# Performance work log

Hardware: AMD Instinct MI355X
Metric: run time of the kernel (lower is better)

## Reference

```python
import jax, jax.numpy as jnp
import numpy as np

N = 8192
IN_F = 128
OUT_F = 128
ALPHA = 0.2  # LeakyReLU negative slope
NEG_INF = -9e15


def setup_inputs() -> dict:
    key = jax.random.key(0)
    k1, k2, k3, k4 = jax.random.split(key, 4)
    h = jax.random.normal(k1, (N, IN_F), dtype=jnp.float32)
    adj = jax.random.randint(k2, (N, N), 0, 2, dtype=jnp.int32)
    # nn.Linear(in, out, bias=False).weight is (out, in); store as (in, out) for h @ W
    W = jax.random.normal(k3, (IN_F, OUT_F), dtype=jnp.float32) * (1.0 / np.sqrt(IN_F))
    # a: (2*out_features, 1), xavier_uniform with gain=1.414
    limit = 1.414 * np.sqrt(6.0 / (2 * OUT_F + 1))
    a = jax.random.uniform(k4, (2 * OUT_F, 1), dtype=jnp.float32, minval=-limit, maxval=limit)
    return {"h": h, "adj": adj, "W": W, "a": a}


def reference(h, adj, W, a):
    Wh = h @ W  # (N, OUT_F)
    a1 = a[:OUT_F, 0]   # score contribution from source node i
    a2 = a[OUT_F:, 0]   # score contribution from target node j
    # e_ij = leakyrelu(Wh_i . a1 + Wh_j . a2) -- avoids the O(N^2 * 2F) concat
    s1 = Wh @ a1  # (N,)
    s2 = Wh @ a2  # (N,)
    e = jax.nn.leaky_relu(s1[:, None] + s2[None, :], negative_slope=ALPHA)  # (N, N)
    masked = jnp.where(adj > 0, e, NEG_INF)
    attention = jax.nn.softmax(masked, axis=1)  # (N, N)
    # dropout is a no-op in eval mode
    h_prime = attention @ Wh  # (N, OUT_F)
    return jax.nn.elu(h_prime)  # concat=True -> ELU
```

## Files before the change

### kernel.cpp

```cpp
#include <hip/hip_runtime.h>
#include <cstdint>
#include <cstddef>


#define NROW 8192
#define FDIM 128

typedef _Float16 f16;
typedef f16 f16x8 __attribute__((ext_vector_type(8)));
typedef float f32x4 __attribute__((ext_vector_type(4)));

#define WS_WHT 0u
#define WS_S12 (2u * 1024u * 1024u)
#define WS_RC  (WS_S12 + 64u * 1024u)
#define WS_EF  (WS_RC + 128u * 1024u)
#define WS_M2  (WS_EF + 64u * 1024u)

__global__ __launch_bounds__(256) void k1_wh(const float* __restrict__ h,
                                             const float* __restrict__ W,
                                             f16* __restrict__ WhT,
                                             unsigned* __restrict__ M2key) {
  __shared__ float hT[128 * 36];
  const int t = (int)threadIdx.x;
  const int rb = (int)blockIdx.x * 32;
  if (blockIdx.x == 0 && t == 0) *M2key = 0u;
  const f32x4* hv = (const f32x4*)(h + (size_t)rb * FDIM);
#pragma unroll
  for (int i = 0; i < 4; ++i) {
    int fidx = t + i * 256;
    f32x4 v = hv[fidx];
    int e0 = fidx * 4;
    int r = e0 >> 7, k = e0 & 127;
    hT[(k + 0) * 36 + r] = v[0];
    hT[(k + 1) * 36 + r] = v[1];
    hT[(k + 2) * 36 + r] = v[2];
    hT[(k + 3) * 36 + r] = v[3];
  }
  __syncthreads();
  const int f = t & 127, rh = t >> 7;
  f32x4 z = {0.f, 0.f, 0.f, 0.f};
  f32x4 acc0 = z, acc1 = z, acc2 = z, acc3 = z;
  for (int k = 0; k < 128; ++k) {
    float w = W[k * FDIM + f];
    const f32x4* hp = (const f32x4*)(hT + k * 36 + rh * 16);
    acc0 += hp[0] * w;
    acc1 += hp[1] * w;
    acc2 += hp[2] * w;
    acc3 += hp[3] * w;
  }
  union { f16 hx[16]; uint4 u[2]; } pk;
#pragma unroll
  for (int q = 0; q < 4; ++q) {
    pk.hx[0 + q]  = (f16)acc0[q];
    pk.hx[4 + q]  = (f16)acc1[q];
    pk.hx[8 + q]  = (f16)acc2[q];
    pk.hx[12 + q] = (f16)acc3[q];
  }
  uint4* dst = (uint4*)(WhT + (size_t)f * NROW + rb + rh * 16);
  dst[0] = pk.u[0];
  dst[1] = pk.u[1];
}

__global__ __launch_bounds__(256) void k1b_s(const f16* __restrict__ WhT,
                                             const float* __restrict__ a,
                                             float2* __restrict__ s12,
                                             unsigned* __restrict__ M2key) {
  int r = (int)blockIdx.x * 256 + (int)threadIdx.x;
  float s1 = 0.f, s2 = 0.f;
  for (int f = 0; f < 128; ++f) {
    float w = (float)WhT[(size_t)f * NROW + r];
    s1 = fmaf(w, a[f], s1);
    s2 = fmaf(w, a[128 + f], s2);
  }
  s12[r] = make_float2(s1, s2);
  float mx = s2;
#pragma unroll
  for (int off = 32; off; off >>= 1) mx = fmaxf(mx, __shfl_xor(mx, off, 64));
  if ((threadIdx.x & 63) == 0) {
    unsigned key = __float_as_uint(mx);
    key = (key & 0x80000000u) ? ~key : (key | 0x80000000u);
    atomicMax(M2key, key);
  }
}

__global__ __launch_bounds__(256) void k1c_prep(const float2* __restrict__ s12,
                                                const unsigned* __restrict__ M2key,
                                                float4* __restrict__ RC,
                                                float2* __restrict__ EF) {
  int j = (int)blockIdx.x * 256 + (int)threadIdx.x;
  unsigned key = *M2key;
  float M2 = (key & 0x80000000u) ? __uint_as_float(key ^ 0x80000000u)
                                 : __uint_as_float(~key);
  float2 s = s12[j];
  float c = s.x + M2;
  c = fmaxf(c, 0.2f * c);
  RC[j] = make_float4(__expf(-s.x), __expf(s.x - c), __expf(0.2f * s.x - c), 0.f);
  EF[j] = make_float2(__expf(s.y), __expf(0.2f * s.y));
}

__global__ __launch_bounds__(512) void k2_main(const int* __restrict__ adj,
                                               const f16* __restrict__ WhT,
                                               const float4* __restrict__ RC,
                                               const float* __restrict__ EF,
                                               float* __restrict__ out) {
  __shared__ __align__(16) f16 whbuf[2][8192];
  __shared__ float dpart[2][32];

  const int tid = (int)threadIdx.x;
  const int L = tid & 63, w = tid >> 6;
  const int mh = w & 1, kh = (w >> 1) & 1, nh = w >> 2;
  const int m = L & 15, kg = L >> 4;
  const int rb = (int)blockIdx.x * 32;
  const int rloc = mh * 16 + m;
  const int row = rb + rloc;
  const int jo = kh * 32 + kg * 8;

  const float4 rc = RC[row];
  const float tau = rc.x, kap1 = rc.y, kap2 = rc.z;

  const int sf0 = tid >> 3;
  const int scc = tid & 7;
  const int stl0 = sf0 * 64 + scc * 8;
  const f16* gp0 = WhT + (size_t)sf0 * NROW + (size_t)((scc ^ (sf0 & 7)) * 8);
  const f16* gp1 = gp0 + (size_t)64 * NROW;

  const int* ap = adj + (size_t)row * NROW + jo;
  const f32x4* ep = (const f32x4*)(EF + 2 * jo);

  uint4 S0 = *(const uint4*)gp0;
  uint4 S1 = *(const uint4*)gp1;
  int4 A0 = *(const int4*)ap;
  int4 A1 = *(const int4*)(ap + 4);
  f32x4 Ev0 = ep[0], Ev1 = ep[1], Ev2 = ep[2], Ev3 = ep[3];

  f32x4 z = {0.f, 0.f, 0.f, 0.f};
  f32x4 acc[4] = {z, z, z, z};
  float dloc = 0.f;

  const int bofs = (nh * 64 + m) * 64 + (((kh * 4 + kg) ^ (m & 7)) * 8);

  for (int t = 0; t < 128; ++t) {
    f16* wb = &whbuf[t & 1][0];
    *(uint4*)(wb + stl0) = S0;
    *(uint4*)(wb + stl0 + 4096) = S1;

    f16x8 af;
    {
      float p;
      p = (Ev0[0] > tau) ? Ev0[0] * kap1 : Ev0[1] * kap2; p = (A0.x > 0) ? p : 0.f; dloc += p; af[0] = (f16)p;
      p = (Ev0[2] > tau) ? Ev0[2] * kap1 : Ev0[3] * kap2; p = (A0.y > 0) ? p : 0.f; dloc += p; af[1] = (f16)p;
      p = (Ev1[0] > tau) ? Ev1[0] * kap1 : Ev1[1] * kap2; p = (A0.z > 0) ? p : 0.f; dloc += p; af[2] = (f16)p;
      p = (Ev1[2] > tau) ? Ev1[2] * kap1 : Ev1[3] * kap2; p = (A0.w > 0) ? p : 0.f; dloc += p; af[3] = (f16)p;
      p = (Ev2[0] > tau) ? Ev2[0] * kap1 : Ev2[1] * kap2; p = (A1.x > 0) ? p : 0.f; dloc += p; af[4] = (f16)p;
      p = (Ev2[2] > tau) ? Ev2[2] * kap1 : Ev2[3] * kap2; p = (A1.y > 0) ? p : 0.f; dloc += p; af[5] = (f16)p;
      p = (Ev3[0] > tau) ? Ev3[0] * kap1 : Ev3[1] * kap2; p = (A1.z > 0) ? p : 0.f; dloc += p; af[6] = (f16)p;
      p = (Ev3[2] > tau) ? Ev3[2] * kap1 : Ev3[3] * kap2; p = (A1.w > 0) ? p : 0.f; dloc += p; af[7] = (f16)p;
    }

    __syncthreads();

    int adv = (t < 127) ? 1 : 0;
    ap += adv * 64;
    ep += adv * 32;
    gp0 += adv * 64;
    gp1 += adv * 64;
    uint4 Sn0 = *(const uint4*)gp0;
    uint4 Sn1 = *(const uint4*)gp1;
    int4 An0 = *(const int4*)ap;
    int4 An1 = *(const int4*)(ap + 4);
    f32x4 En0 = ep[0], En1 = ep[1], En2 = ep[2], En3 = ep[3];

    const f16* wbB = wb + bofs;
    f16x8 b0 = *(const f16x8*)(wbB);
    f16x8 b1 = *(const f16x8*)(wbB + 1024);
    f16x8 b2 = *(const f16x8*)(wbB + 2048);
    f16x8 b3 = *(const f16x8*)(wbB + 3072);
    acc[0] = __builtin_amdgcn_mfma_f32_16x16x32_f16(af, b0, acc[0], 0, 0, 0);
    acc[1] = __builtin_amdgcn_mfma_f32_16x16x32_f16(af, b1, acc[1], 0, 0, 0);
    acc[2] = __builtin_amdgcn_mfma_f32_16x16x32_f16(af, b2, acc[2], 0, 0, 0);
    acc[3] = __builtin_amdgcn_mfma_f32_16x16x32_f16(af, b3, acc[3], 0, 0, 0);

    S0 = Sn0; S1 = Sn1; A0 = An0; A1 = An1;
    Ev0 = En0; Ev1 = En1; Ev2 = En2; Ev3 = En3;
  }

  dloc += __shfl_xor(dloc, 16, 64);
  dloc += __shfl_xor(dloc, 32, 64);
  if (nh == 0 && kg == 0) dpart[kh][rloc] = dloc;
  __syncthreads();

  float* red = (float*)&whbuf[0][0];
  const int q4 = (nh * 2 + mh) * 4;
  if (kh == 1) {
#pragma unroll
    for (int nt = 0; nt < 4; ++nt)
#pragma unroll
      for (int e = 0; e < 4; ++e)
        red[(q4 + nt) * 288 + (kg * 4 + e) * 18 + m] = acc[nt][e];
  }
  __syncthreads();
  if (kh == 0) {
    float inv0[4];
#pragma unroll
    for (int e = 0; e < 4; ++e) {
      int rr = mh * 16 + kg * 4 + e;
      inv0[e] = 1.0f / (dpart[0][rr] + dpart[1][rr]);
    }
#pragma unroll
    for (int nt = 0; nt < 4; ++nt) {
#pragma unroll
      for (int e = 0; e < 4; ++e) {
        float x = (acc[nt][e] + red[(q4 + nt) * 288 + (kg * 4 + e) * 18 + m]) * inv0[e];
        float r = x > 0.f ? x : expm1f(x);
        out[(size_t)(rb + mh * 16 + kg * 4 + e) * FDIM + nh * 64 + nt * 16 + m] = r;
      }
    }
  }
}

extern "C" void kernel_launch(void* const* d_in, const int* in_sizes, int n_in,
                              void* d_out, int out_size, void* d_ws, size_t ws_size,
                              hipStream_t stream) {
  const float* h = (const float*)d_in[0];
  const int* adj = (const int*)d_in[1];
  const float* W = (const float*)d_in[2];
  const float* a = (const float*)d_in[3];
  float* out = (float*)d_out;
  char* ws = (char*)d_ws;
  f16* WhT = (f16*)(ws + WS_WHT);
  float2* s12 = (float2*)(ws + WS_S12);
  float4* RC = (float4*)(ws + WS_RC);
  float2* EF = (float2*)(ws + WS_EF);
  unsigned* M2 = (unsigned*)(ws + WS_M2);

  k1_wh<<<dim3(256), dim3(256), 0, stream>>>(h, W, WhT, M2);
  k1b_s<<<dim3(32), dim3(256), 0, stream>>>(WhT, a, s12, M2);
  k1c_prep<<<dim3(32), dim3(256), 0, stream>>>(s12, M2, RC, EF);
  k2_main<<<dim3(256), dim3(512), 0, stream>>>(adj, WhT, RC, (const float*)EF, out);
}
```

Baseline: 533.2 us.

## Split-K main attention kernel over column chunks with 32x32 MFMA and combine pass

Rewrites the main attention-times-Wh kernel so each wavefront owns a 32-row block and one of S column chunks. It reads Wh from a pre-packed MFMA-ready fp16 layout straight from global memory instead of staging it through LDS with barriers, and uses 32x32x16 MFMAs. Partial numerators and denominators go to workspace and a new combine kernel normalizes them and applies ELU. This raises parallelism beyond 256 blocks and removes LDS sync, at the cost of partial-sum traffic, an extra launch and repeated global reads of the packed Wh. k1b_s is also split across four feature groups for more blocks.

Result: faster. 449.8 us (-15.6%).

```diff
diff --git a/kernel.cpp b/kernel.cpp
--- a/kernel.cpp
+++ b/kernel.cpp
@@ -9,16 +9,20 @@
 typedef _Float16 f16;
 typedef f16 f16x8 __attribute__((ext_vector_type(8)));
 typedef float f32x4 __attribute__((ext_vector_type(4)));
+typedef float f32x16 __attribute__((ext_vector_type(16)));
 
 #define WS_WHT 0u
-#define WS_S12 (2u * 1024u * 1024u)
-#define WS_RC  (WS_S12 + 64u * 1024u)
-#define WS_EF  (WS_RC + 128u * 1024u)
-#define WS_M2  (WS_EF + 64u * 1024u)
+#define WS_BP  (2u*1024u*1024u)
+#define WS_S12 (4u*1024u*1024u)
+#define WS_RC  (WS_S12 + 64u*1024u)
+#define WS_EF  (WS_RC + 128u*1024u)
+#define WS_M2  (WS_EF + 64u*1024u)
+#define WS_PWS (WS_M2 + 4u*1024u)
 
 __global__ __launch_bounds__(256) void k1_wh(const float* __restrict__ h,
                                              const float* __restrict__ W,
                                              f16* __restrict__ WhT,
+                                             f16* __restrict__ Bp,
                                              unsigned* __restrict__ M2key) {
   __shared__ float hT[128 * 36];
   const int t = (int)threadIdx.x;
@@ -59,27 +63,40 @@
   uint4* dst = (uint4*)(WhT + (size_t)f * NROW + rb + rh * 16);
   dst[0] = pk.u[0];
   dst[1] = pk.u[1];
+  f16* bdst = Bp + ((size_t)((blockIdx.x * 2 + rh) * 4 + (f >> 5)) * 64 + (f & 31)) * 8;
+  *(uint4*)bdst = pk.u[0];
+  *(uint4*)(bdst + 256) = pk.u[1];
 }
 
 __global__ __launch_bounds__(256) void k1b_s(const f16* __restrict__ WhT,
                                              const float* __restrict__ a,
                                              float2* __restrict__ s12,
                                              unsigned* __restrict__ M2key) {
-  int r = (int)blockIdx.x * 256 + (int)threadIdx.x;
+  __shared__ float part[2][4][64];
+  const int l = (int)threadIdx.x & 63;
+  const int fc = (int)threadIdx.x >> 6;
+  const int r = (int)blockIdx.x * 64 + l;
   float s1 = 0.f, s2 = 0.f;
-  for (int f = 0; f < 128; ++f) {
+  for (int f = fc * 32; f < fc * 32 + 32; ++f) {
     float w = (float)WhT[(size_t)f * NROW + r];
     s1 = fmaf(w, a[f], s1);
     s2 = fmaf(w, a[128 + f], s2);
   }
-  s12[r] = make_float2(s1, s2);
-  float mx = s2;
-#pragma unroll
-  for (int off = 32; off; off >>= 1) mx = fmaxf(mx, __shfl_xor(mx, off, 64));
-  if ((threadIdx.x & 63) == 0) {
-    unsigned key = __float_as_uint(mx);
-    key = (key & 0x80000000u) ? ~key : (key | 0x80000000u);
-    atomicMax(M2key, key);
+  part[0][fc][l] = s1;
+  part[1][fc][l] = s2;
+  __syncthreads();
+  if (fc == 0) {
+    s1 = part[0][0][l] + part[0][1][l] + part[0][2][l] + part[0][3][l];
+    s2 = part[1][0][l] + part[1][1][l] + part[1][2][l] + part[1][3][l];
+    s12[r] = make_float2(s1, s2);
+    float mx = s2;
+#pragma unroll
+    for (int off = 32; off; off >>= 1) mx = fmaxf(mx, __shfl_xor(mx, off, 64));
+    if (l == 0) {
+      unsigned key = __float_as_uint(mx);
+      key = (key & 0x80000000u) ? ~key : (key | 0x80000000u);
+      atomicMax(M2key, key);
+    }
   }
 }
 
@@ -98,124 +115,127 @@
   EF[j] = make_float2(__expf(s.y), __expf(0.2f * s.y));
 }
 
-__global__ __launch_bounds__(512) void k2_main(const int* __restrict__ adj,
-                                               const f16* __restrict__ WhT,
+__global__ __launch_bounds__(256) void k2_main(const int* __restrict__ adj,
+                                               const f16* __restrict__ Bp,
                                                const float4* __restrict__ RC,
                                                const float* __restrict__ EF,
-                                               float* __restrict__ out) {
-  __shared__ __align__(16) f16 whbuf[2][8192];
-  __shared__ float dpart[2][32];
-
+                                               float* __restrict__ Pws,
+                                               float* __restrict__ Dws,
+                                               int jspan) {
   const int tid = (int)threadIdx.x;
   const int L = tid & 63, w = tid >> 6;
-  const int mh = w & 1, kh = (w >> 1) & 1, nh = w >> 2;
-  const int m = L & 15, kg = L >> 4;
-  const int rb = (int)blockIdx.x * 32;
-  const int rloc = mh * 16 + m;
-  const int row = rb + rloc;
-  const int jo = kh * 32 + kg * 8;
+  const int wid = (int)blockIdx.x * 4 + w;
+  const int rg = wid & 255;
+  const int c = wid >> 8;
+  const int rb = rg * 32;
+  const int m = L & 31, kb = L >> 5;
+  const int row = rb + m;
+  const int j0 = c * jspan;
+  const int niter = jspan >> 5;
 
   const float4 rc = RC[row];
   const float tau = rc.x, kap1 = rc.y, kap2 = rc.z;
 
-  const int sf0 = tid >> 3;
-  const int scc = tid & 7;
-  const int stl0 = sf0 * 64 + scc * 8;
-  const f16* gp0 = WhT + (size_t)sf0 * NROW + (size_t)((scc ^ (sf0 & 7)) * 8);
-  const f16* gp1 = gp0 + (size_t)64 * NROW;
-
-  const int* ap = adj + (size_t)row * NROW + jo;
-  const f32x4* ep = (const f32x4*)(EF + 2 * jo);
-
-  uint4 S0 = *(const uint4*)gp0;
-  uint4 S1 = *(const uint4*)gp1;
+  const int* ap = adj + (size_t)row * NROW + j0 + kb * 8;
+  const f32x4* ep = (const f32x4*)(EF + 2 * (j0 + kb * 8));
+  const f16* bp = Bp + (size_t)(j0 >> 4) * 2048 + L * 8;
+
   int4 A0 = *(const int4*)ap;
   int4 A1 = *(const int4*)(ap + 4);
-  f32x4 Ev0 = ep[0], Ev1 = ep[1], Ev2 = ep[2], Ev3 = ep[3];
-
-  f32x4 z = {0.f, 0.f, 0.f, 0.f};
-  f32x4 acc[4] = {z, z, z, z};
+  int4 A2 = *(const int4*)(ap + 16);
+  int4 A3 = *(const int4*)(ap + 20);
+  f32x4 E0 = ep[0], E1 = ep[1], E2 = ep[2], E3 = ep[3];
+  f32x4 E4 = ep[8], E5 = ep[9], E6 = ep[10], E7 = ep[11];
+
+  f32x16 zz = {0.f};
+  f32x16 acc[4] = {zz, zz, zz, zz};
   float dloc = 0.f;
 
-  const int bofs = (nh * 64 + m) * 64 + (((kh * 4 + kg) ^ (m & 7)) * 8);
-
-  for (int t = 0; t < 128; ++t) {
-    f16* wb = &whbuf[t & 1][0];
-    *(uint4*)(wb + stl0) = S0;
-    *(uint4*)(wb + stl0 + 4096) = S1;
-
-    f16x8 af;
+  for (int it = 0; it < niter; ++it) {
+    const f16* bt = bp + (size_t)it * 4096;
+    f16x8 B00 = *(const f16x8*)(bt);
+    f16x8 B01 = *(const f16x8*)(bt + 512);
+    f16x8 B02 = *(const f16x8*)(bt + 1024);
+    f16x8 B03 = *(const f16x8*)(bt + 1536);
+    f16x8 B10 = *(const f16x8*)(bt + 2048);
+    f16x8 B11 = *(const f16x8*)(bt + 2560);
+    f16x8 B12 = *(const f16x8*)(bt + 3072);
+    f16x8 B13 = *(const f16x8*)(bt + 3584);
+
+    f16x8 af0, af1;
     {
       float p;
-      p = (Ev0[0] > tau) ? Ev0[0] * kap1 : Ev0[1] * kap2; p = (A0.x > 0) ? p : 0.f; dloc += p; af[0] = (f16)p;
-      p = (Ev0[2] > tau) ? Ev0[2] * kap1 : Ev0[3] * kap2; p = (A0.y > 0) ? p : 0.f; dloc += p; af[1] = (f16)p;
-      p = (Ev1[0] > tau) ? Ev1[0] * kap1 : Ev1[1] * kap2; p = (A0.z > 0) ? p : 0.f; dloc += p; af[2] = (f16)p;
-      p = (Ev1[2] > tau) ? Ev1[2] * kap1 : Ev1[3] * kap2; p = (A0.w > 0) ? p : 0.f; dloc += p; af[3] = (f16)p;
-      p = (Ev2[0] > tau) ? Ev2[0] * kap1 : Ev2[1] * kap2; p = (A1.x > 0) ? p : 0.f; dloc += p; af[4] = (f16)p;
-      p = (Ev2[2] > tau) ? Ev2[2] * kap1 : Ev2[3] * kap2; p = (A1.y > 0) ? p : 0.f; dloc += p; af[5] = (f16)p;
-      p = (Ev3[0] > tau) ? Ev3[0] * kap1 : Ev3[1] * kap2; p = (A1.z > 0) ? p : 0.f; dloc += p; af[6] = (f16)p;
-      p = (Ev3[2] > tau) ? Ev3[2] * kap1 : Ev3[3] * kap2; p = (A1.w > 0) ? p : 0.f; dloc += p; af[7] = (f16)p;
+      p = (E0[0] > tau) ? E0[0] * kap1 : E0[1] * kap2; p = (A0.x > 0) ? p : 0.f; dloc += p; af0[0] = (f16)p;
+      p = (E0[2] > tau) ? E0[2] * kap1 : E0[3] * kap2; p = (A0.y > 0) ? p : 0.f; dloc += p; af0[1] = (f16)p;
+      p = (E1[0] > tau) ? E1[0] * kap1 : E1[1] * kap2; p = (A0.z > 0) ? p : 0.f; dloc += p; af0[2] = (f16)p;
+      p = (E1[2] > tau) ? E1[2] * kap1 : E1[3] * kap2; p = (A0.w > 0) ? p : 0.f; dloc += p; af0[3] = (f16)p;
+      p = (E2[0] > tau) ? E2[0] * kap1 : E2[1] * kap2; p = (A1.x > 0) ? p : 0.f; dloc += p; af0[4] = (f16)p;
+      p = (E2[2] > tau) ? E2[2] * kap1 : E2[3] * kap2; p = (A1.y > 0) ? p : 0.f; dloc += p; af0[5] = (f16)p;
+      p = (E3[0] > tau) ? E3[0] * kap1 : E3[1] * kap2; p = (A1.z > 0) ? p : 0.f; dloc += p; af0[6] = (f16)p;
+      p = (E3[2] > tau) ? E3[2] * kap1 : E3[3] * kap2; p = (A1.w > 0) ? p : 0.f; dloc += p; af0[7] = (f16)p;
+      p = (E4[0] > tau) ? E4[0] * kap1 : E4[1] * kap2; p = (A2.x > 0) ? p : 0.f; dloc += p; af1[0] = (f16)p;
+      p = (E4[2] > tau) ? E4[2] * kap1 : E4[3] * kap2; p = (A2.y > 0) ? p : 0.f; dloc += p; af1[1] = (f16)p;
+      p = (E5[0] > tau) ? E5[0] * kap1 : E5[1] * kap2; p = (A2.z > 0) ? p : 0.f; dloc += p; af1[2] = (f16)p;
+      p = (E5[2] > tau) ? E5[2] * kap1 : E5[3] * kap2; p = (A2.w > 0) ? p : 0.f; dloc += p; af1[3] = (f16)p;
+      p = (E6[0] > tau) ? E6[0] * kap1 : E6[1] * kap2; p = (A3.x > 0) ? p : 0.f; dloc += p; af1[4] = (f16)p;
+      p = (E6[2] > tau) ? E6[2] * kap1 : E6[3] * kap2; p = (A3.y > 0) ? p : 0.f; dloc += p; af1[5] = (f16)p;
+      p = (E7[0] > tau) ? E7[0] * kap1 : E7[1] * kap2; p = (A3.z > 0) ? p : 0.f; dloc += p; af1[6] = (f16)p;
+      p = (E7[2] > tau) ? E7[2] * kap1 : E7[3] * kap2; p = (A3.w > 0) ? p : 0.f; dloc += p; af1[7] = (f16)p;
     }
 
-    __syncthreads();
-
-    int adv = (t < 127) ? 1 : 0;
-    ap += adv * 64;
-    ep += adv * 32;
-    gp0 += adv * 64;
-    gp1 += adv * 64;
-    uint4 Sn0 = *(const uint4*)gp0;
-    uint4 Sn1 = *(const uint4*)gp1;
-    int4 An0 = *(const int4*)ap;
-    int4 An1 = *(const int4*)(ap + 4);
-    f32x4 En0 = ep[0], En1 = ep[1], En2 = ep[2], En3 = ep[3];
-
-    const f16* wbB = wb + bofs;
-    f16x8 b0 = *(const f16x8*)(wbB);
-    f16x8 b1 = *(const f16x8*)(wbB + 1024);
-    f16x8 b2 = *(const f16x8*)(wbB + 2048);
-    f16x8 b3 = *(const f16x8*)(wbB + 3072);
-    acc[0] = __builtin_amdgcn_mfma_f32_16x16x32_f16(af, b0, acc[0], 0, 0, 0);
-    acc[1] = __builtin_amdgcn_mfma_f32_16x16x32_f16(af, b1, acc[1], 0, 0, 0);
-    acc[2] = __builtin_amdgcn_mfma_f32_16x16x32_f16(af, b2, acc[2], 0, 0, 0);
-    acc[3] = __builtin_amdgcn_mfma_f32_16x16x32_f16(af, b3, acc[3], 0, 0, 0);
-
-    S0 = Sn0; S1 = Sn1; A0 = An0; A1 = An1;
-    Ev0 = En0; Ev1 = En1; Ev2 = En2; Ev3 = En3;
-  }
-
-  dloc += __shfl_xor(dloc, 16, 64);
+    int adv = (it < niter - 1) ? 1 : 0;
+    ap += adv * 32;
+    ep += adv * 16;
+    A0 = *(const int4*)ap;
+    A1 = *(const int4*)(ap + 4);
+    A2 = *(const int4*)(ap + 16);
+    A3 = *(const int4*)(ap + 20);
+    E0 = ep[0]; E1 = ep[1]; E2 = ep[2]; E3 = ep[3];
+    E4 = ep[8]; E5 = ep[9]; E6 = ep[10]; E7 = ep[11];
+
+    acc[0] = __builtin_amdgcn_mfma_f32_32x32x16_f16(af0, B00, acc[0], 0, 0, 0);
+    acc[1] = __builtin_amdgcn_mfma_f32_32x32x16_f16(af0, B01, acc[1], 0, 0, 0);
+    acc[2] = __builtin_amdgcn_mfma_f32_32x32x16_f16(af0, B02, acc[2], 0, 0, 0);
+    acc[3] = __builtin_amdgcn_mfma_f32_32x32x16_f16(af0, B03, acc[3], 0, 0, 0);
+    acc[0] = __builtin_amdgcn_mfma_f32_32x32x16_f16(af1, B10, acc[0], 0, 0, 0);
+    acc[1] = __builtin_amdgcn_mfma_f32_32x32x16_f16(af1, B11, acc[1], 0, 0, 0);
+    acc[2] = __builtin_amdgcn_mfma_f32_32x32x16_f16(af1, B12, acc[2], 0, 0, 0);
+    acc[3] = __builtin_amdgcn_mfma_f32_32x32x16_f16(af1, B13, acc[3], 0, 0, 0);
+  }
+
   dloc += __shfl_xor(dloc, 32, 64);
-  if (nh == 0 && kg == 0) dpart[kh][rloc] = dloc;
-  __syncthreads();
-
-  float* red = (float*)&whbuf[0][0];
-  const int q4 = (nh * 2 + mh) * 4;
-  if (kh == 1) {
-#pragma unroll
-    for (int nt = 0; nt < 4; ++nt)
-#pragma unroll
-      for (int e = 0; e < 4; ++e)
-        red[(q4 + nt) * 288 + (kg * 4 + e) * 18 + m] = acc[nt][e];
-  }
-  __syncthreads();
-  if (kh == 0) {
-    float inv0[4];
-#pragma unroll
-    for (int e = 0; e < 4; ++e) {
-      int rr = mh * 16 + kg * 4 + e;
-      inv0[e] = 1.0f / (dpart[0][rr] + dpart[1][rr]);
+  if (L < 32) Dws[(size_t)c * NROW + row] = dloc;
+
+  float* P = Pws + ((size_t)c * NROW + rb) * FDIM + (L & 31);
+#pragma unroll
+  for (int nt = 0; nt < 4; ++nt) {
+#pragma unroll
+    for (int reg = 0; reg < 16; ++reg) {
+      int rr = (reg & 3) + 8 * (reg >> 2) + 4 * kb;
+      P[(size_t)rr * FDIM + nt * 32] = acc[nt][reg];
     }
-#pragma unroll
-    for (int nt = 0; nt < 4; ++nt) {
-#pragma unroll
-      for (int e = 0; e < 4; ++e) {
-        float x = (acc[nt][e] + red[(q4 + nt) * 288 + (kg * 4 + e) * 18 + m]) * inv0[e];
-        float r = x > 0.f ? x : expm1f(x);
-        out[(size_t)(rb + mh * 16 + kg * 4 + e) * FDIM + nh * 64 + nt * 16 + m] = r;
-      }
-    }
-  }
+  }
+}
+
+__global__ __launch_bounds__(256) void k3_comb(const float* __restrict__ Pws,
+                                               const float* __restrict__ Dws,
+                                               float* __restrict__ out, int S) {
+  int g = (int)blockIdx.x * 256 + (int)threadIdx.x;
+  int r = g >> 5, f4 = g & 31;
+  f32x4 s = {0.f, 0.f, 0.f, 0.f};
+  float den = 0.f;
+  for (int c2 = 0; c2 < S; ++c2) {
+    s += *(const f32x4*)(Pws + ((size_t)c2 * NROW + r) * FDIM + f4 * 4);
+    den += Dws[(size_t)c2 * NROW + r];
+  }
+  float inv = 1.0f / den;
+  f32x4 o;
+#pragma unroll
+  for (int e = 0; e < 4; ++e) {
+    float x = s[e] * inv;
+    o[e] = x > 0.f ? x : expm1f(x);
+  }
+  *(f32x4*)(out + (size_t)r * FDIM + f4 * 4) = o;
 }
 
 extern "C" void kernel_launch(void* const* d_in, const int* in_sizes, int n_in,
@@ -228,13 +248,21 @@
   float* out = (float*)d_out;
   char* ws = (char*)d_ws;
   f16* WhT = (f16*)(ws + WS_WHT);
+  f16* Bp = (f16*)(ws + WS_BP);
   float2* s12 = (float2*)(ws + WS_S12);
   float4* RC = (float4*)(ws + WS_RC);
   float2* EF = (float2*)(ws + WS_EF);
   unsigned* M2 = (unsigned*)(ws + WS_M2);
 
-  k1_wh<<<dim3(256), dim3(256), 0, stream>>>(h, W, WhT, M2);
-  k1b_s<<<dim3(32), dim3(256), 0, stream>>>(WhT, a, s12, M2);
+  const size_t partial_bytes = (size_t)NROW * FDIM * 4;
+  int S = (ws_size >= WS_PWS + 8 * partial_bytes + 8 * NROW * 4) ? 8 : 2;
+  float* Pws = (float*)(ws + WS_PWS);
+  float* Dws = (float*)(ws + WS_PWS + (size_t)S * partial_bytes);
+  int jspan = NROW / S;
+
+  k1_wh<<<dim3(256), dim3(256), 0, stream>>>(h, W, WhT, Bp, M2);
+  k1b_s<<<dim3(128), dim3(256), 0, stream>>>(WhT, a, s12, M2);
   k1c_prep<<<dim3(32), dim3(256), 0, stream>>>(s12, M2, RC, EF);
-  k2_main<<<dim3(256), dim3(512), 0, stream>>>(adj, WhT, RC, (const float*)EF, out);
-}
+  k2_main<<<dim3(64 * S), dim3(256), 0, stream>>>(adj, Bp, RC, (const float*)EF, Pws, Dws, jspan);
+  k3_comb<<<dim3(1024), dim3(256), 0, stream>>>(Pws, Dws, out, S);
+}
```
